# Optimization experiments

Measured on AMD Instinct MI355X. Metric: run time of the kernel, lower is better.

The kernel has to match this reference:

```python
import jax, jax.numpy as jnp
import numpy as np


def _inst(Xs, idx):
    # Xs: list of [N_type, D] feature tables, one per metapath position.
    # idx: [N, K, P] int indices. Returns max-pooled instance vectors [N, K, D].
    v = Xs[0][idx[..., 0]]
    for p in range(1, len(Xs)):
        v = jnp.maximum(v, Xs[p][idx[..., p]])
    return v


def _instance_attn(h, inst, W, a):
    # h: [N, D] target features; inst: [N, K, D]; W: [H, D, D]; a: [H, D].
    hi = jnp.einsum('nd,hde->hne', h, W)               # [H, N, D]
    hv = jnp.einsum('nkd,hde->hnke', inst, W)          # [H, N, K, D]
    e = jax.nn.leaky_relu(
        jnp.einsum('hnke,he->hnk', hv + hi[:, :, None, :], a), 0.2)
    alpha = jax.nn.softmax(e, axis=2)                  # softmax over K instances
    out = jnp.einsum('hnk,hnke->ne', alpha, hv)
    return out / W.shape[0]                            # mean over heads


def _metapath_attn(Hs, W, b, q):
    Hstk = jnp.stack(Hs)                               # [P, N, D]
    sem = jnp.tanh(Hstk @ W + b).mean(axis=1)          # [P, D]
    beta = jax.nn.softmax(jnp.sum(jnp.tanh(sem) * q, axis=1), axis=0)  # [P]
    return jnp.einsum('p,pnd->nd', beta, Hstk), beta


def setup_inputs() -> dict:
    N, D, K, H = 2048, 256, 20, 4
    key = jax.random.key(0)
    ks = iter(jax.random.split(key, 40))
    nrm = lambda shape, s=1.0: jax.random.normal(next(ks), shape, jnp.float32) * s
    ridx = lambda shape: jax.random.randint(next(ks), shape, 0, N, jnp.int32)
    w_s = 1.0 / np.sqrt(D).astype(np.float32)
    inp = {
        'X_drug': nrm((N, D)), 'X_dis': nrm((N, D)), 'X_gene': nrm((N, D)),
        'idx_rdr': ridx((N, K, 3)), 'idx_rdgdr': ridx((N, K, 5)),
        'idx_dgd': ridx((N, K, 3)), 'idx_drd': ridx((N, K, 3)),
        'idx_drrd': ridx((N, K, 4)), 'idx_gdrdg': ridx((N, K, 5)),
    }
    for mp in ['rdr', 'rdgdr', 'dgd', 'drd', 'drrd', 'gdrdg']:
        inp['W_' + mp] = nrm((H, D, D), w_s)
        inp['a_' + mp] = nrm((H, D), 0.01)
    for t in ['drug', 'dis', 'gene']:
        inp['Wm_' + t] = nrm((D, D), w_s)
        inp['bm_' + t] = jnp.zeros((D,), jnp.float32)
        inp['qm_' + t] = nrm((D,), 0.01)
    return inp


def reference(X_drug, X_dis, X_gene,
              idx_rdr, idx_rdgdr, idx_dgd, idx_drd, idx_drrd, idx_gdrdg,
              W_rdr, a_rdr, W_rdgdr, a_rdgdr, W_dgd, a_dgd, W_drd, a_drd,
              W_drrd, a_drrd, W_gdrdg, a_gdrdg,
              Wm_drug, bm_drug, qm_drug, Wm_dis, bm_dis, qm_dis,
              Wm_gene, bm_gene, qm_gene):
    # Drug metapaths: RDR, RDGDR
    H_rdr = _instance_attn(X_drug, _inst([X_drug, X_dis, X_drug], idx_rdr), W_rdr, a_rdr)
    H_rdgdr = _instance_attn(X_drug, _inst([X_drug, X_dis, X_gene, X_dis, X_drug], idx_rdgdr), W_rdgdr, a_rdgdr)
    H_drug, beta_drug = _metapath_attn([H_rdr, H_rdgdr], Wm_drug, bm_drug, qm_drug)
    # Disease metapaths: DGD, DRD, DRRD
    H_dgd = _instance_attn(X_dis, _inst([X_dis, X_gene, X_dis], idx_dgd), W_dgd, a_dgd)
    H_drd = _instance_attn(X_dis, _inst([X_dis, X_drug, X_dis], idx_drd), W_drd, a_drd)
    H_drrd = _instance_attn(X_dis, _inst([X_dis, X_drug, X_drug, X_dis], idx_drrd), W_drrd, a_drrd)
    H_dis, beta_dis = _metapath_attn([H_dgd, H_drd, H_drrd], Wm_dis, bm_dis, qm_dis)
    # Gene metapath: GDRDG
    H_gdrdg = _instance_attn(X_gene, _inst([X_gene, X_dis, X_drug, X_dis, X_gene], idx_gdrdg), W_gdrdg, a_gdrdg)
    H_gene, beta_gene = _metapath_attn([H_gdrdg], Wm_gene, bm_gene, qm_gene)
    return H_drug, H_dis, H_gene, beta_drug, beta_dis, beta_gene
```

## Files before the change

### kernel.cpp

```cpp
#include <hip/hip_runtime.h>
#include <math.h>

#define NN 2048
#define DD 256
#define KK 20
#define HH 4

typedef short short8 __attribute__((ext_vector_type(8)));
typedef float f32x4  __attribute__((ext_vector_type(4)));
typedef _Float16 half8 __attribute__((ext_vector_type(8)));
typedef _Float16 h2    __attribute__((ext_vector_type(2)));

#if defined(__has_builtin)
#  if __has_builtin(__builtin_amdgcn_fdot2)
#    define HAS_FDOT2 1
#  else
#    define HAS_FDOT2 0
#  endif
#else
#  define HAS_FDOT2 0
#endif

struct AllMP  { const unsigned short* xs[6][5]; const int* idx[6]; const unsigned short* xt[6]; int P[6]; };
struct SixPtr { const float* p[6]; };
struct SemB   { const unsigned short* Wmt[6]; const float* bm[6]; };

__device__ inline float wsum(float v){
  #pragma unroll
  for (int o=32;o;o>>=1) v += __shfl_xor(v,o);
  return v;
}
__device__ inline float wmax(float v){
  #pragma unroll
  for (int o=32;o;o>>=1) v = fmaxf(v,__shfl_xor(v,o));
  return v;
}
__device__ inline float gsum16(float v){
  #pragma unroll
  for (int o=8;o;o>>=1) v += __shfl_xor(v,o);
  return v;
}
__device__ inline unsigned short f2h(float x){
  return __builtin_bit_cast(unsigned short, (_Float16)x);
}
__device__ inline float h2f(unsigned short u){
  return (float)__builtin_bit_cast(_Float16, u);
}
__device__ inline h2 bch2(unsigned int u){ return __builtin_bit_cast(h2, u); }
__device__ inline unsigned int bcu(h2 v){ return __builtin_bit_cast(unsigned int, v); }
__device__ inline h2 packh2(float a, float b){ h2 r; r[0]=(_Float16)a; r[1]=(_Float16)b; return r; }
__device__ inline h2 hmax2(h2 a, h2 b){
  unsigned int d, ua = bcu(a), ub = bcu(b);
  asm("v_pk_max_f16 %0, %1, %2" : "=v"(d) : "v"(ua), "v"(ub));
  return bch2(d);
}
__device__ inline float dot2(h2 a, h2 b, float c){
#if HAS_FDOT2
  return __builtin_amdgcn_fdot2(a, b, c, false);
#else
  return c + (float)a[0]*(float)b[0] + (float)a[1]*(float)b[1];
#endif
}
__device__ inline void glds16(const void* g, void* l){
  __builtin_amdgcn_global_load_lds(
    (const __attribute__((address_space(1))) unsigned int*)g,
    (__attribute__((address_space(3))) unsigned int*)l, 16, 0, 0);
}

__launch_bounds__(256)
__global__ void prep_kernel(SixPtr W, SixPtr a, SixPtr Xp, SixPtr Wm3,
                            float* __restrict__ wa, unsigned short* __restrict__ Xh,
                            unsigned short* __restrict__ Wt, unsigned short* __restrict__ Wmt,
                            float* __restrict__ zero_base, int zero_cnt){
  __shared__ unsigned short T_s[64][68];
  int b = blockIdx.x;
  const int t = threadIdx.x;

  if (b < 24){
    if (b == 0){
      for (int i=t;i<zero_cnt;i+=256) zero_base[i] = 0.f;
    }
    const int m = b >> 2;
    const int local = ((b & 3) << 8) | t;
    const int h = local >> 8, d = local & 255;
    const float4* wrow = (const float4*)(W.p[m] + (size_t)(h*DD + d)*DD);
    const float4* av   = (const float4*)(a.p[m] + h*DD);
    float acc = 0.f;
    #pragma unroll 8
    for (int e=0;e<64;e++){
      float4 wv = wrow[e], xv = av[e];
      acc += wv.x*xv.x + wv.y*xv.y + wv.z*xv.z + wv.w*xv.w;
    }
    wa[m*1024 + local] = acc;
    return;
  }
  b -= 24;
  if (b < 1536){
    int gid = b*256 + t;
    int tb  = gid >> 17;
    int off = gid & 131071;
    float4 v = ((const float4*)Xp.p[tb])[off];
    ushort4 o = { f2h(v.x), f2h(v.y), f2h(v.z), f2h(v.w) };
    ((ushort4*)(Xh + (size_t)tb*NN*DD))[off] = o;
    return;
  }
  b -= 1536;
  const float* src; unsigned short* ob; int R, C, r0, c0;
  if (b < 384){
    int m = b/64, rem = b%64;
    src = W.p[m]; ob = Wt + (size_t)m*256*1024;
    R = 1024; C = 256; r0 = (rem>>2)*64; c0 = (rem&3)*64;
  } else {
    int bb = b-384;
    int m = bb/16, rem = bb%16;
    src = Wm3.p[m]; ob = Wmt + (size_t)m*256*256;
    R = 256; C = 256; r0 = (rem>>2)*64; c0 = (rem&3)*64;
  }
  {
    const int rr = t>>4, cc = (t&15)*4;
    #pragma unroll
    for (int i=0;i<4;i++){
      float4 v = *(const float4*)(src + (size_t)(r0+rr+i*16)*C + c0 + cc);
      T_s[cc+0][rr+i*16]=f2h(v.x);
      T_s[cc+1][rr+i*16]=f2h(v.y);
      T_s[cc+2][rr+i*16]=f2h(v.z);
      T_s[cc+3][rr+i*16]=f2h(v.w);
    }
    __syncthreads();
    const int cr = t>>4, rc = (t&15)*4;
    #pragma unroll
    for (int i=0;i<4;i++){
      int c = c0 + cr + i*16;
      ushort4 v = { T_s[cr+i*16][rc+0], T_s[cr+i*16][rc+1],
                    T_s[cr+i*16][rc+2], T_s[cr+i*16][rc+3] };
      int col = (r0 + rc) ^ ((c&7)<<3);
      *(ushort4*)(ob + (size_t)c*R + col) = v;
    }
  }
}

template<int P>
__device__ inline void gather_dot(const AllMP& mp, int m, int wu, int l, int g, int j,
                                  const int* __restrict__ gidx, unsigned int (*inst_u)[128],
                                  const h2* wh, float sg, float (*e_s)[HH]){
  #pragma unroll
  for (int kk=0; kk<5; kk++){
    const int k = wu*5 + kk;
    const unsigned short* rp[P];
    #pragma unroll
    for (int p=0;p<P;p++){
      int id = gidx[k*P + p];
      rp[p] = mp.xs[m][p] + (size_t)id*DD;
    }
    uint2 r = *(const uint2*)(rp[0] + 4*l);
    h2 v0 = bch2(r.x), v1 = bch2(r.y);
    #pragma unroll
    for (int p=1;p<P;p++){
      uint2 u = *(const uint2*)(rp[p] + 4*l);
      v0 = hmax2(v0, bch2(u.x));
      v1 = hmax2(v1, bch2(u.y));
    }
    *(uint2*)&inst_u[k][2*l] = make_uint2(bcu(v0), bcu(v1));
  }
  #pragma unroll
  for (int kk=0; kk<5; kk++){
    const int k = wu*5 + kk;
    float pr = 0.f;
    #pragma unroll
    for (int c=0;c<4;c++){
      uint2 rr = *(const uint2*)&inst_u[k][2*(j+16*c)];
      pr = dot2(bch2(rr.x), wh[2*c+0], pr);
      pr = dot2(bch2(rr.y), wh[2*c+1], pr);
    }
    pr = gsum16(pr);
    if (j==0){
      float logit = pr + sg;
      e_s[k][g] = (logit>0.f) ? logit : 0.2f*logit;
    }
  }
}

__launch_bounds__(256)
__global__ void inst_attn_kernel(AllMP mp, const float* __restrict__ wa_all,
                                 unsigned short* __restrict__ ctxh){
  __shared__ unsigned int inst_u[KK][128];
  __shared__ float e_s[KK][HH];
  __shared__ float alpha_s[KK][HH];

  const int m = blockIdx.y;
  const int n = blockIdx.x;
  const int t = threadIdx.x;
  const int l = t & 63;
  const int wu = __builtin_amdgcn_readfirstlane(t >> 6);
  const int g = l >> 4;
  const int j = l & 15;
  const int P = mp.P[m];
  const int* __restrict__ gidx = mp.idx[m] + (size_t)n*(KK*P);

  h2 wh[8];
  {
    const float4* wab = (const float4*)(wa_all + m*1024 + g*256);
    float4 w0 = wab[j], w1 = wab[j+16], w2 = wab[j+32], w3 = wab[j+48];
    wh[0]=packh2(w0.x,w0.y); wh[1]=packh2(w0.z,w0.w);
    wh[2]=packh2(w1.x,w1.y); wh[3]=packh2(w1.z,w1.w);
    wh[4]=packh2(w2.x,w2.y); wh[5]=packh2(w2.z,w2.w);
    wh[6]=packh2(w3.x,w3.y); wh[7]=packh2(w3.z,w3.w);
  }

  float sg;
  {
    const unsigned short* xb = mp.xt[m] + (size_t)n*DD;
    float p_ = 0.f;
    #pragma unroll
    for (int c=0;c<4;c++){
      uint2 rr = *(const uint2*)(xb + 4*(j+16*c));
      p_ = dot2(bch2(rr.x), wh[2*c+0], p_);
      p_ = dot2(bch2(rr.y), wh[2*c+1], p_);
    }
    sg = gsum16(p_);
  }

  switch(P){
    case 3: gather_dot<3>(mp,m,wu,l,g,j,gidx,inst_u,wh,sg,e_s); break;
    case 4: gather_dot<4>(mp,m,wu,l,g,j,gidx,inst_u,wh,sg,e_s); break;
    default: gather_dot<5>(mp,m,wu,l,g,j,gidx,inst_u,wh,sg,e_s); break;
  }
  __syncthreads();

  {
    float x  = (l<KK) ? e_s[l][wu] : -INFINITY;
    float mx = wmax(x);
    float pv = (l<KK) ? expf(x-mx) : 0.f;
    float sm = wsum(pv);
    if (l<KK) alpha_s[l][wu] = pv/sm;
  }
  __syncthreads();

  const unsigned short* ih = (const unsigned short*)&inst_u[0][0];
  float c0=0,c1=0,c2=0,c3=0;
  #pragma unroll
  for (int k=0;k<KK;k++){
    float4 al = *(const float4*)&alpha_s[k][0];
    float iv = h2f(ih[k*DD + t]);
    c0 += al.x*iv; c1 += al.y*iv; c2 += al.z*iv; c3 += al.w*iv;
  }
  unsigned short* cb = ctxh + ((size_t)m*NN + n)*1024;
  const int ts = t ^ ((n&7)<<3);
  cb[0*DD+ts]=f2h(c0); cb[1*DD+ts]=f2h(c1); cb[2*DD+ts]=f2h(c2); cb[3*DD+ts]=f2h(c3);
}

__launch_bounds__(256)
__global__ void gemm_kernel(const unsigned short* __restrict__ ctxh,
                            const unsigned short* __restrict__ Wt,
                            unsigned short* __restrict__ Hmp){
  __shared__ unsigned short A_s[64][64];
  __shared__ unsigned short B_s[64][64];
  const int m  = blockIdx.z;
  const int n0 = blockIdx.x*64, c0 = blockIdx.y*64;
  const int t  = threadIdx.x;
  const int l  = t & 63;
  const int wid  = t >> 6;
  const int wrow = wid & 1, wcol = wid >> 1;
  const unsigned short* Abase = ctxh + (size_t)m*NN*1024;
  const unsigned short* Bbase = Wt   + (size_t)m*256*1024;

  f32x4 acc[2][2] = {};
  const int row8 = l>>3, seg = l&7;

  for (int k0=0; k0<1024; k0+=64){
    #pragma unroll
    for (int i=0;i<2;i++){
      const int r = wid*16 + i*8;
      glds16(Abase + (size_t)(n0+r+row8)*1024 + k0 + seg*8, &A_s[r][0]);
      glds16(Bbase + (size_t)(c0+r+row8)*1024 + k0 + seg*8, &B_s[r][0]);
    }
    __syncthreads();
    #pragma unroll
    for (int kf=0;kf<2;kf++){
      half8 a[2], b[2];
      const int s = kf*4 + (l>>4);
      #pragma unroll
      for (int mr=0;mr<2;mr++){
        const int row = wrow*32 + mr*16 + (l&15);
        a[mr] = __builtin_bit_cast(half8, *(const short8*)&A_s[row][(s ^ (row&7))*8]);
      }
      #pragma unroll
      for (int nr=0;nr<2;nr++){
        const int col = wcol*32 + nr*16 + (l&15);
        b[nr] = __builtin_bit_cast(half8, *(const short8*)&B_s[col][(s ^ (col&7))*8]);
      }
      #pragma unroll
      for (int mr=0;mr<2;mr++)
        #pragma unroll
        for (int nr=0;nr<2;nr++)
          acc[mr][nr] = __builtin_amdgcn_mfma_f32_16x16x32_f16(a[mr], b[nr], acc[mr][nr], 0,0,0);
    }
    __syncthreads();
  }
  unsigned short* out = Hmp + (size_t)m*NN*DD;
  #pragma unroll
  for (int mr=0;mr<2;mr++){
    const int rbase = n0 + wrow*32 + mr*16 + (l>>4)*4;
    #pragma unroll
    for (int nr=0;nr<2;nr++){
      const int col = c0 + wcol*32 + nr*16 + (l&15);
      #pragma unroll
      for (int r=0;r<4;r++){
        const int rw = rbase + r;
        out[(size_t)rw*DD + (col ^ ((rw&7)<<3))] = f2h(acc[mr][nr][r]*0.25f);
      }
    }
  }
}

__launch_bounds__(256)
__global__ void sem_kernel(const unsigned short* __restrict__ Hmp, SemB sb,
                           float* __restrict__ sem_sum){
  __shared__ unsigned short A_s[64][256];
  __shared__ unsigned short B_s[64][256];
  const int m  = blockIdx.z;
  const int n0 = blockIdx.x*64, c0 = blockIdx.y*64;
  const int t  = threadIdx.x, l = t & 63, wid = t >> 6;
  const int wrow = wid & 1, wcol = wid >> 1;
  const unsigned short* Ab = Hmp + (size_t)m*NN*DD;
  const unsigned short* Bb = sb.Wmt[m];

  const int row2 = l>>5, seg = l&31;
  #pragma unroll
  for (int i=0;i<8;i++){
    const int r = wid*16 + i*2;
    glds16(Ab + (size_t)(n0+r+row2)*DD + seg*8, &A_s[r][0]);
    glds16(Bb + (size_t)(c0+r+row2)*DD + seg*8, &B_s[r][0]);
  }
  __syncthreads();

  f32x4 acc[2][2] = {};
  #pragma unroll
  for (int kf=0; kf<8; kf++){
    const int s = kf*4 + (l>>4);
    half8 a[2], b[2];
    #pragma unroll
    for (int mr=0;mr<2;mr++){
      int row = wrow*32 + mr*16 + (l&15);
      int ss = (s&24) | ((s&7)^(row&7));
      a[mr] = __builtin_bit_cast(half8, *(const short8*)((const char*)&A_s[0][0] + row*512 + ss*16));
    }
    #pragma unroll
    for (int nr=0;nr<2;nr++){
      int row = wcol*32 + nr*16 + (l&15);
      int ss = (s&24) | ((s&7)^(row&7));
      b[nr] = __builtin_bit_cast(half8, *(const short8*)((const char*)&B_s[0][0] + row*512 + ss*16));
    }
    #pragma unroll
    for (int mr=0;mr<2;mr++)
      #pragma unroll
      for (int nr=0;nr<2;nr++)
        acc[mr][nr] = __builtin_amdgcn_mfma_f32_16x16x32_f16(a[mr], b[nr], acc[mr][nr], 0,0,0);
  }

  #pragma unroll
  for (int nr=0;nr<2;nr++){
    const int col = c0 + wcol*32 + nr*16 + (l&15);
    float b = sb.bm[m][col];
    float sv = 0.f;
    #pragma unroll
    for (int mr=0;mr<2;mr++)
      #pragma unroll
      for (int r=0;r<4;r++)
        sv += tanhf(acc[mr][nr][r] + b);
    sv += __shfl_xor(sv,16);
    sv += __shfl_xor(sv,32);
    if (l < 16) atomicAdd(&sem_sum[m*DD + col], sv);
  }
}

struct TypeInfo { const float* qm; float* sem; int P; int beta_off; };
__global__ void beta_kernel(TypeInfo ti0, TypeInfo ti1, TypeInfo ti2,
                            float* __restrict__ out_beta, float* __restrict__ beta_ws){
  TypeInfo ti = (blockIdx.x==0) ? ti0 : (blockIdx.x==1) ? ti1 : ti2;
  const int t = threadIdx.x;
  __shared__ float red[4];
  __shared__ float logits[3];
  float q = ti.qm[t];
  for (int p=0;p<ti.P;p++){
    float sm = ti.sem[p*DD + t] * (1.0f/NN);
    float v = tanhf(sm)*q;
    v = wsum(v);
    if ((t&63)==0) red[t>>6] = v;
    __syncthreads();
    if (t==0) logits[p] = red[0]+red[1]+red[2]+red[3];
    __syncthreads();
  }
  if (t==0){
    float mx = -INFINITY;
    for (int p=0;p<ti.P;p++) mx = fmaxf(mx, logits[p]);
    float s = 0.f, e[3];
    for (int p=0;p<ti.P;p++){ e[p] = expf(logits[p]-mx); s += e[p]; }
    for (int p=0;p<ti.P;p++){
      float b = e[p]/s;
      out_beta[ti.beta_off + p] = b;
      beta_ws[blockIdx.x*3 + p] = b;
    }
  }
}

__global__ void combine_kernel(const unsigned short* __restrict__ Hmp,
                               const float* __restrict__ beta_ws,
                               float* __restrict__ out){
  const int type = blockIdx.y;
  const int start = (type==0) ? 0 : (type==1) ? 2 : 5;
  const int P = (type==0) ? 2 : (type==1) ? 3 : 1;
  const int n = blockIdx.x;
  const int d = threadIdx.x;
  const int ds = d ^ ((n&7)<<3);
  const unsigned short* base = Hmp + ((size_t)start*NN + n)*DD + ds;
  float acc = 0.f;
  for (int p=0;p<P;p++) acc += beta_ws[type*3+p]*h2f(base[(size_t)p*NN*DD]);
  out[((size_t)type*NN + n)*DD + d] = acc;
}

extern "C" void kernel_launch(void* const* d_in, const int* in_sizes, int n_in,
                              void* d_out, int out_size, void* d_ws, size_t ws_size,
                              hipStream_t stream) {
  SixPtr Xp; Xp.p[0]=(const float*)d_in[0]; Xp.p[1]=(const float*)d_in[1]; Xp.p[2]=(const float*)d_in[2];
  for (int i=3;i<6;i++) Xp.p[i]=Xp.p[0];

  SixPtr Wl, al;
  for (int m=0;m<6;m++){ Wl.p[m] = (const float*)d_in[9+2*m]; al.p[m] = (const float*)d_in[10+2*m]; }
  const float* Wm_[3]; const float* bm_[3]; const float* qm_[3];
  for (int tt=0;tt<3;tt++){
    Wm_[tt] = (const float*)d_in[21+3*tt];
    bm_[tt] = (const float*)d_in[22+3*tt];
    qm_[tt] = (const float*)d_in[23+3*tt];
  }
  SixPtr Wm3; for (int i=0;i<6;i++) Wm3.p[i] = Wm_[i<3?i:0];

  char* ws = (char*)d_ws;
  float* wa_all  = (float*)ws;                               ws += 6*1024*4;
  float* sem_sum = (float*)ws;                               ws += 6*DD*4;
  float* beta_ws = (float*)ws;                               ws += 16*4;
  unsigned short* Hmp  = (unsigned short*)ws;                ws += (size_t)6*NN*DD*2;
  unsigned short* Wt   = (unsigned short*)ws;                ws += (size_t)6*256*1024*2;
  unsigned short* Wmt  = (unsigned short*)ws;                ws += (size_t)3*256*256*2;
  unsigned short* Xh   = (unsigned short*)ws;                ws += (size_t)3*NN*DD*2;
  unsigned short* ctxh = (unsigned short*)ws;

  AllMP mp;
  for (int m=0;m<6;m++) mp.idx[m] = (const int*)d_in[3+m];
  const int P_[6] = {3,5,3,3,4,5};
  for (int m=0;m<6;m++) mp.P[m] = P_[m];
  const int xt_t[6] = {0,0,1,1,1,2};
  const int gp_t[6][5] = {
    {0,1,0,0,0}, {0,1,2,1,0}, {1,2,1,1,1},
    {1,0,1,1,1}, {1,0,0,1,1}, {2,1,0,1,2}};
  for (int m=0;m<6;m++){
    mp.xt[m] = Xh + (size_t)xt_t[m]*NN*DD;
    for (int p=0;p<5;p++) mp.xs[m][p] = Xh + (size_t)gp_t[m][p]*NN*DD;
  }

  SemB sb;
  const int type_of[6] = {0,0,1,1,1,2};
  for (int m=0;m<6;m++){
    sb.Wmt[m] = Wmt + (size_t)type_of[m]*256*256;
    sb.bm[m]  = bm_[type_of[m]];
  }

  prep_kernel<<<dim3(24+1536+384+48),dim3(256),0,stream>>>(
      Wl, al, Xp, Wm3, wa_all, Xh, Wt, Wmt, sem_sum, 6*DD+16);

  inst_attn_kernel<<<dim3(NN,6),dim3(256),0,stream>>>(mp, wa_all, ctxh);
  gemm_kernel<<<dim3(32,4,6),dim3(256),0,stream>>>(ctxh, Wt, Hmp);
  sem_kernel<<<dim3(32,4,6),dim3(256),0,stream>>>(Hmp, sb, sem_sum);

  float* out = (float*)d_out;
  TypeInfo t0{qm_[0], sem_sum + 0*DD, 2, 0};
  TypeInfo t1{qm_[1], sem_sum + 2*DD, 3, 2};
  TypeInfo t2{qm_[2], sem_sum + 5*DD, 1, 5};
  beta_kernel<<<dim3(3),dim3(256),0,stream>>>(t0, t1, t2, out + (size_t)3*NN*DD, beta_ws);

  combine_kernel<<<dim3(NN,3),dim3(256),0,stream>>>(Hmp, beta_ws, out);
}
```

Measured before the change: 104.0 us.

## Use one-wave instance attention, double-buffer GEMM, fuse beta into combine

The instance-attention kernel becomes a single 64-thread wave per node that keeps gathered instances in registers and computes the softmax per lane. This removes the block-level barriers and the separate alpha pass. The GEMM now double-buffers its LDS tiles and raises wave priority around the MFMAs so loads overlap compute. The beta softmax kernel is folded into the combine kernel, which now handles 4 rows per block and recomputes beta in every block, saving one launch at the cost of redundant tanh reductions and higher register pressure in the attention kernel.

```diff
diff --git a/kernel.cpp b/kernel.cpp
--- a/kernel.cpp
+++ b/kernel.cpp
@@ -28,11 +28,6 @@
 __device__ inline float wsum(float v){
   #pragma unroll
   for (int o=32;o;o>>=1) v += __shfl_xor(v,o);
-  return v;
-}
-__device__ inline float wmax(float v){
-  #pragma unroll
-  for (int o=32;o;o>>=1) v = fmaxf(v,__shfl_xor(v,o));
   return v;
 }
 __device__ inline float gsum16(float v){
@@ -140,121 +135,130 @@
 }
 
 template<int P>
-__device__ inline void gather_dot(const AllMP& mp, int m, int wu, int l, int g, int j,
-                                  const int* __restrict__ gidx, unsigned int (*inst_u)[128],
-                                  const h2* wh, float sg, float (*e_s)[HH]){
-  #pragma unroll
-  for (int kk=0; kk<5; kk++){
-    const int k = wu*5 + kk;
-    const unsigned short* rp[P];
-    #pragma unroll
-    for (int p=0;p<P;p++){
-      int id = gidx[k*P + p];
-      rp[p] = mp.xs[m][p] + (size_t)id*DD;
-    }
-    uint2 r = *(const uint2*)(rp[0] + 4*l);
-    h2 v0 = bch2(r.x), v1 = bch2(r.y);
-    #pragma unroll
-    for (int p=1;p<P;p++){
-      uint2 u = *(const uint2*)(rp[p] + 4*l);
-      v0 = hmax2(v0, bch2(u.x));
-      v1 = hmax2(v1, bch2(u.y));
-    }
-    *(uint2*)&inst_u[k][2*l] = make_uint2(bcu(v0), bcu(v1));
-  }
-  #pragma unroll
-  for (int kk=0; kk<5; kk++){
-    const int k = wu*5 + kk;
-    float pr = 0.f;
-    #pragma unroll
-    for (int c=0;c<4;c++){
-      uint2 rr = *(const uint2*)&inst_u[k][2*(j+16*c)];
-      pr = dot2(bch2(rr.x), wh[2*c+0], pr);
-      pr = dot2(bch2(rr.y), wh[2*c+1], pr);
-    }
-    pr = gsum16(pr);
-    if (j==0){
-      float logit = pr + sg;
-      e_s[k][g] = (logit>0.f) ? logit : 0.2f*logit;
-    }
-  }
-}
-
-__launch_bounds__(256)
-__global__ void inst_attn_kernel(AllMP mp, const float* __restrict__ wa_all,
+__device__ inline void inst_core(const AllMP& mp, int m, int n, int l,
+                                 const float* __restrict__ wa_all,
+                                 unsigned int (*inst_lds)[128], float (*alpha_lds)[4],
                                  unsigned short* __restrict__ ctxh){
-  __shared__ unsigned int inst_u[KK][128];
-  __shared__ float e_s[KK][HH];
-  __shared__ float alpha_s[KK][HH];
-
-  const int m = blockIdx.y;
-  const int n = blockIdx.x;
-  const int t = threadIdx.x;
-  const int l = t & 63;
-  const int wu = __builtin_amdgcn_readfirstlane(t >> 6);
   const int g = l >> 4;
   const int j = l & 15;
-  const int P = mp.P[m];
   const int* __restrict__ gidx = mp.idx[m] + (size_t)n*(KK*P);
 
   h2 wh[8];
   {
     const float4* wab = (const float4*)(wa_all + m*1024 + g*256);
-    float4 w0 = wab[j], w1 = wab[j+16], w2 = wab[j+32], w3 = wab[j+48];
-    wh[0]=packh2(w0.x,w0.y); wh[1]=packh2(w0.z,w0.w);
-    wh[2]=packh2(w1.x,w1.y); wh[3]=packh2(w1.z,w1.w);
-    wh[4]=packh2(w2.x,w2.y); wh[5]=packh2(w2.z,w2.w);
-    wh[6]=packh2(w3.x,w3.y); wh[7]=packh2(w3.z,w3.w);
+    #pragma unroll
+    for (int c=0;c<4;c++){
+      float4 wv = wab[j + 16*c];
+      wh[2*c]   = packh2(wv.x, wv.y);
+      wh[2*c+1] = packh2(wv.z, wv.w);
+    }
   }
 
   float sg;
   {
-    const unsigned short* xb = mp.xt[m] + (size_t)n*DD;
+    const uint2* xb = (const uint2*)(mp.xt[m] + (size_t)n*DD);
     float p_ = 0.f;
     #pragma unroll
     for (int c=0;c<4;c++){
-      uint2 rr = *(const uint2*)(xb + 4*(j+16*c));
+      uint2 rr = xb[j + 16*c];
       p_ = dot2(bch2(rr.x), wh[2*c+0], p_);
       p_ = dot2(bch2(rr.y), wh[2*c+1], p_);
     }
     sg = gsum16(p_);
   }
 
-  switch(P){
-    case 3: gather_dot<3>(mp,m,wu,l,g,j,gidx,inst_u,wh,sg,e_s); break;
-    case 4: gather_dot<4>(mp,m,wu,l,g,j,gidx,inst_u,wh,sg,e_s); break;
-    default: gather_dot<5>(mp,m,wu,l,g,j,gidx,inst_u,wh,sg,e_s); break;
-  }
-  __syncthreads();
-
-  {
-    float x  = (l<KK) ? e_s[l][wu] : -INFINITY;
-    float mx = wmax(x);
-    float pv = (l<KK) ? expf(x-mx) : 0.f;
-    float sm = wsum(pv);
-    if (l<KK) alpha_s[l][wu] = pv/sm;
-  }
-  __syncthreads();
-
-  const unsigned short* ih = (const unsigned short*)&inst_u[0][0];
-  float c0=0,c1=0,c2=0,c3=0;
+  unsigned int v0[KK], v1[KK];
   #pragma unroll
   for (int k=0;k<KK;k++){
-    float4 al = *(const float4*)&alpha_s[k][0];
-    float iv = h2f(ih[k*DD + t]);
-    c0 += al.x*iv; c1 += al.y*iv; c2 += al.z*iv; c3 += al.w*iv;
-  }
+    h2 a, bb;
+    {
+      int id = gidx[k*P];
+      const uint2* rp = (const uint2*)(mp.xs[m][0] + (size_t)id*DD);
+      uint2 r = rp[l];
+      a = bch2(r.x); bb = bch2(r.y);
+    }
+    #pragma unroll
+    for (int p=1;p<P;p++){
+      int id = gidx[k*P+p];
+      const uint2* rp = (const uint2*)(mp.xs[m][p] + (size_t)id*DD);
+      uint2 u = rp[l];
+      a = hmax2(a, bch2(u.x)); bb = hmax2(bb, bch2(u.y));
+    }
+    v0[k] = bcu(a); v1[k] = bcu(bb);
+    *(uint2*)&inst_lds[k][2*l] = make_uint2(v0[k], v1[k]);
+  }
+
+  float e[KK];
+  #pragma unroll
+  for (int k=0;k<KK;k++){
+    float pr = 0.f;
+    #pragma unroll
+    for (int c=0;c<4;c++){
+      uint2 rr = *(const uint2*)&inst_lds[k][2*(j+16*c)];
+      pr = dot2(bch2(rr.x), wh[2*c+0], pr);
+      pr = dot2(bch2(rr.y), wh[2*c+1], pr);
+    }
+    pr = gsum16(pr);
+    float logit = pr + sg;
+    e[k] = (logit>0.f) ? logit : 0.2f*logit;
+  }
+
+  float mx = e[0];
+  #pragma unroll
+  for (int k=1;k<KK;k++) mx = fmaxf(mx, e[k]);
+  float s = 0.f;
+  #pragma unroll
+  for (int k=0;k<KK;k++){ e[k] = __expf(e[k]-mx); s += e[k]; }
+  float inv = 1.0f/s;
+  #pragma unroll
+  for (int k=0;k<KK;k++) e[k] *= inv;
+  if (j==0){
+    #pragma unroll
+    for (int k=0;k<KK;k++) alpha_lds[k][g] = e[k];
+  }
+
+  float c[4][4] = {};
+  #pragma unroll
+  for (int k=0;k<KK;k++){
+    float4 af = *(const float4*)&alpha_lds[k][0];
+    h2 x0 = bch2(v0[k]), x1 = bch2(v1[k]);
+    float f0=(float)x0[0], f1=(float)x0[1], f2=(float)x1[0], f3=(float)x1[1];
+    c[0][0]+=af.x*f0; c[0][1]+=af.x*f1; c[0][2]+=af.x*f2; c[0][3]+=af.x*f3;
+    c[1][0]+=af.y*f0; c[1][1]+=af.y*f1; c[1][2]+=af.y*f2; c[1][3]+=af.y*f3;
+    c[2][0]+=af.z*f0; c[2][1]+=af.z*f1; c[2][2]+=af.z*f2; c[2][3]+=af.z*f3;
+    c[3][0]+=af.w*f0; c[3][1]+=af.w*f1; c[3][2]+=af.w*f2; c[3][3]+=af.w*f3;
+  }
+
   unsigned short* cb = ctxh + ((size_t)m*NN + n)*1024;
-  const int ts = t ^ ((n&7)<<3);
-  cb[0*DD+ts]=f2h(c0); cb[1*DD+ts]=f2h(c1); cb[2*DD+ts]=f2h(c2); cb[3*DD+ts]=f2h(c3);
+  const int col = (4*l) ^ ((n&7)<<3);
+  #pragma unroll
+  for (int h=0;h<4;h++){
+    ushort4 o = { f2h(c[h][0]), f2h(c[h][1]), f2h(c[h][2]), f2h(c[h][3]) };
+    *(ushort4*)(cb + h*DD + col) = o;
+  }
+}
+
+__launch_bounds__(64)
+__global__ void inst_attn_kernel(AllMP mp, const float* __restrict__ wa_all,
+                                 unsigned short* __restrict__ ctxh){
+  __shared__ unsigned int inst_lds[KK][128];
+  __shared__ float alpha_lds[KK][4];
+  const int m = blockIdx.y;
+  const int n = blockIdx.x;
+  const int l = threadIdx.x;
+  switch(mp.P[m]){
+    case 3: inst_core<3>(mp,m,n,l,wa_all,inst_lds,alpha_lds,ctxh); break;
+    case 4: inst_core<4>(mp,m,n,l,wa_all,inst_lds,alpha_lds,ctxh); break;
+    default: inst_core<5>(mp,m,n,l,wa_all,inst_lds,alpha_lds,ctxh); break;
+  }
 }
 
 __launch_bounds__(256)
 __global__ void gemm_kernel(const unsigned short* __restrict__ ctxh,
                             const unsigned short* __restrict__ Wt,
                             unsigned short* __restrict__ Hmp){
-  __shared__ unsigned short A_s[64][64];
-  __shared__ unsigned short B_s[64][64];
+  __shared__ unsigned short A_s[2][64][64];
+  __shared__ unsigned short B_s[2][64][64];
   const int m  = blockIdx.z;
   const int n0 = blockIdx.x*64, c0 = blockIdx.y*64;
   const int t  = threadIdx.x;
@@ -267,14 +271,29 @@
   f32x4 acc[2][2] = {};
   const int row8 = l>>3, seg = l&7;
 
-  for (int k0=0; k0<1024; k0+=64){
+  {
     #pragma unroll
     for (int i=0;i<2;i++){
       const int r = wid*16 + i*8;
-      glds16(Abase + (size_t)(n0+r+row8)*1024 + k0 + seg*8, &A_s[r][0]);
-      glds16(Bbase + (size_t)(c0+r+row8)*1024 + k0 + seg*8, &B_s[r][0]);
-    }
-    __syncthreads();
+      glds16(Abase + (size_t)(n0+r+row8)*1024 + 0 + seg*8, &A_s[0][r][0]);
+      glds16(Bbase + (size_t)(c0+r+row8)*1024 + 0 + seg*8, &B_s[0][r][0]);
+    }
+  }
+  __syncthreads();
+
+  #pragma unroll 2
+  for (int it=0; it<16; it++){
+    const int buf = it&1;
+    if (it<15){
+      const int k0 = (it+1)*64;
+      #pragma unroll
+      for (int i=0;i<2;i++){
+        const int r = wid*16 + i*8;
+        glds16(Abase + (size_t)(n0+r+row8)*1024 + k0 + seg*8, &A_s[buf^1][r][0]);
+        glds16(Bbase + (size_t)(c0+r+row8)*1024 + k0 + seg*8, &B_s[buf^1][r][0]);
+      }
+    }
+    __builtin_amdgcn_s_setprio(1);
     #pragma unroll
     for (int kf=0;kf<2;kf++){
       half8 a[2], b[2];
@@ -282,12 +301,12 @@
       #pragma unroll
       for (int mr=0;mr<2;mr++){
         const int row = wrow*32 + mr*16 + (l&15);
-        a[mr] = __builtin_bit_cast(half8, *(const short8*)&A_s[row][(s ^ (row&7))*8]);
+        a[mr] = __builtin_bit_cast(half8, *(const short8*)&A_s[buf][row][(s ^ (row&7))*8]);
       }
       #pragma unroll
       for (int nr=0;nr<2;nr++){
         const int col = wcol*32 + nr*16 + (l&15);
-        b[nr] = __builtin_bit_cast(half8, *(const short8*)&B_s[col][(s ^ (col&7))*8]);
+        b[nr] = __builtin_bit_cast(half8, *(const short8*)&B_s[buf][col][(s ^ (col&7))*8]);
       }
       #pragma unroll
       for (int mr=0;mr<2;mr++)
@@ -295,8 +314,10 @@
         for (int nr=0;nr<2;nr++)
           acc[mr][nr] = __builtin_amdgcn_mfma_f32_16x16x32_f16(a[mr], b[nr], acc[mr][nr], 0,0,0);
     }
+    __builtin_amdgcn_s_setprio(0);
     __syncthreads();
   }
+
   unsigned short* out = Hmp + (size_t)m*NN*DD;
   #pragma unroll
   for (int mr=0;mr<2;mr++){
@@ -374,49 +395,66 @@
   }
 }
 
-struct TypeInfo { const float* qm; float* sem; int P; int beta_off; };
-__global__ void beta_kernel(TypeInfo ti0, TypeInfo ti1, TypeInfo ti2,
-                            float* __restrict__ out_beta, float* __restrict__ beta_ws){
-  TypeInfo ti = (blockIdx.x==0) ? ti0 : (blockIdx.x==1) ? ti1 : ti2;
-  const int t = threadIdx.x;
-  __shared__ float red[4];
-  __shared__ float logits[3];
-  float q = ti.qm[t];
-  for (int p=0;p<ti.P;p++){
-    float sm = ti.sem[p*DD + t] * (1.0f/NN);
-    float v = tanhf(sm)*q;
-    v = wsum(v);
-    if ((t&63)==0) red[t>>6] = v;
-    __syncthreads();
-    if (t==0) logits[p] = red[0]+red[1]+red[2]+red[3];
-    __syncthreads();
-  }
-  if (t==0){
-    float mx = -INFINITY;
-    for (int p=0;p<ti.P;p++) mx = fmaxf(mx, logits[p]);
-    float s = 0.f, e[3];
-    for (int p=0;p<ti.P;p++){ e[p] = expf(logits[p]-mx); s += e[p]; }
-    for (int p=0;p<ti.P;p++){
-      float b = e[p]/s;
-      out_beta[ti.beta_off + p] = b;
-      beta_ws[blockIdx.x*3 + p] = b;
-    }
-  }
-}
-
+__launch_bounds__(256)
 __global__ void combine_kernel(const unsigned short* __restrict__ Hmp,
-                               const float* __restrict__ beta_ws,
+                               const float* __restrict__ sem_sum,
+                               const float* __restrict__ qm0, const float* __restrict__ qm1,
+                               const float* __restrict__ qm2,
                                float* __restrict__ out){
   const int type = blockIdx.y;
   const int start = (type==0) ? 0 : (type==1) ? 2 : 5;
   const int P = (type==0) ? 2 : (type==1) ? 3 : 1;
-  const int n = blockIdx.x;
-  const int d = threadIdx.x;
-  const int ds = d ^ ((n&7)<<3);
-  const unsigned short* base = Hmp + ((size_t)start*NN + n)*DD + ds;
-  float acc = 0.f;
-  for (int p=0;p<P;p++) acc += beta_ws[type*3+p]*h2f(base[(size_t)p*NN*DD]);
-  out[((size_t)type*NN + n)*DD + d] = acc;
+  const float* qm = (type==0) ? qm0 : (type==1) ? qm1 : qm2;
+  const int t = threadIdx.x;
+  __shared__ float red[3][4];
+  __shared__ float beta_s[3];
+
+  float q = qm[t];
+  #pragma unroll
+  for (int p=0;p<3;p++){
+    if (p < P){
+      float sm = sem_sum[(start+p)*DD + t] * (1.0f/NN);
+      float v = wsum(tanhf(sm)*q);
+      if ((t&63)==0) red[p][t>>6] = v;
+    }
+  }
+  __syncthreads();
+  if (t==0){
+    float logits[3], e[3];
+    float mx = -INFINITY;
+    #pragma unroll
+    for (int p=0;p<3;p++){
+      if (p < P){
+        logits[p] = red[p][0]+red[p][1]+red[p][2]+red[p][3];
+        mx = fmaxf(mx, logits[p]);
+      }
+    }
+    float s = 0.f;
+    #pragma unroll
+    for (int p=0;p<3;p++){
+      if (p < P){ e[p] = __expf(logits[p]-mx); s += e[p]; }
+    }
+    #pragma unroll
+    for (int p=0;p<3;p++)
+      if (p < P) beta_s[p] = e[p]/s;
+  }
+  __syncthreads();
+
+  if (blockIdx.x==0 && t<P)
+    out[(size_t)3*NN*DD + start + t] = beta_s[t];
+
+  const int n0 = blockIdx.x*4;
+  #pragma unroll
+  for (int r=0;r<4;r++){
+    const int n = n0 + r;
+    const int ds = t ^ ((n&7)<<3);
+    const unsigned short* base = Hmp + ((size_t)start*NN + n)*DD + ds;
+    float acc = 0.f;
+    #pragma unroll
+    for (int p=0;p<3;p++)
+      if (p < P) acc += beta_s[p]*h2f(base[(size_t)p*NN*DD]);
+    out[((size_t)type*NN + n)*DD + t] = acc;
+  }
 }
 
 extern "C" void kernel_launch(void* const* d_in, const int* in_sizes, int n_in,
@@ -438,7 +476,6 @@
   char* ws = (char*)d_ws;
   float* wa_all  = (float*)ws;                               ws += 6*1024*4;
   float* sem_sum = (float*)ws;                               ws += 6*DD*4;
-  float* beta_ws = (float*)ws;                               ws += 16*4;
   unsigned short* Hmp  = (unsigned short*)ws;                ws += (size_t)6*NN*DD*2;
   unsigned short* Wt   = (unsigned short*)ws;                ws += (size_t)6*256*1024*2;
   unsigned short* Wmt  = (unsigned short*)ws;                ws += (size_t)3*256*256*2;
@@ -466,17 +503,12 @@
   }
 
   prep_kernel<<<dim3(24+1536+384+48),dim3(256),0,stream>>>(
-      Wl, al, Xp, Wm3, wa_all, Xh, Wt, Wmt, sem_sum, 6*DD+16);
-
-  inst_attn_kernel<<<dim3(NN,6),dim3(256),0,stream>>>(mp, wa_all, ctxh);
+      Wl, al, Xp, Wm3, wa_all, Xh, Wt, Wmt, sem_sum, 6*DD);
+
+  inst_attn_kernel<<<dim3(NN,6),dim3(64),0,stream>>>(mp, wa_all, ctxh);
   gemm_kernel<<<dim3(32,4,6),dim3(256),0,stream>>>(ctxh, Wt, Hmp);
   sem_kernel<<<dim3(32,4,6),dim3(256),0,stream>>>(Hmp, sb, sem_sum);
 
   float* out = (float*)d_out;
-  TypeInfo t0{qm_[0], sem_sum + 0*DD, 2, 0};
-  TypeInfo t1{qm_[1], sem_sum + 2*DD, 3, 2};
-  TypeInfo t2{qm_[2], sem_sum + 5*DD, 1, 5};
-  beta_kernel<<<dim3(3),dim3(256),0,stream>>>(t0, t1, t2, out + (size_t)3*NN*DD, beta_ws);
-
-  combine_kernel<<<dim3(NN,3),dim3(256),0,stream>>>(Hmp, beta_ws, out);
-}
+  combine_kernel<<<dim3(NN/4,3),dim3(256),0,stream>>>(Hmp, sem_sum, qm_[0], qm_[1], qm_[2], out);
+}
```

Result: faster. 91.21 us (-12.3%).
